# Kernel optimization log

Hardware: AMD Instinct MI355X
Metric: run time of the kernel (lower is better)

## Reference

```python
import jax, jax.numpy as jnp
import numpy as np

N = 100000   # nodes
E = 1600000  # edges
IN, H1, H2, OUT = 512, 64, 16, 40


def setup_inputs() -> dict:
    key = jax.random.key(0)
    ks = jax.random.split(key, 8)
    x = jax.random.normal(ks[0], (N, IN), jnp.float32)
    edge_index = jax.random.randint(ks[1], (2, E), 0, N, dtype=jnp.int64)

    def glorot(k, i, o):
        s = np.sqrt(6.0 / (i + o)).astype(np.float32)
        return jax.random.uniform(k, (i, o), jnp.float32, -s, s)

    return dict(
        x=x, edge_index=edge_index,
        W1=glorot(ks[2], IN, H1), b1=jnp.zeros((H1,), jnp.float32),
        W2=glorot(ks[3], H1, H2), b2=jnp.zeros((H2,), jnp.float32),
        W3=glorot(ks[4], H2, OUT), b3=jnp.zeros((OUT,), jnp.float32),
    )


def _gcn_conv(x, src, dst, W, b):
    # PyG GCNConv: x' = D^{-1/2} (A + I) D^{-1/2} (x W) + b
    h = x @ W                                   # [N, F_out]
    n = x.shape[0]
    deg = jnp.zeros((n,), h.dtype).at[dst].add(1.0) + 1.0   # self-loop adds 1
    dinv = jax.lax.rsqrt(deg)                   # deg >= 1 always
    norm = dinv[src] * dinv[dst]                # [E]
    msg = h[src] * norm[:, None]                # gather + scale  [E, F_out]
    out = jnp.zeros_like(h).at[dst].add(msg)    # scatter-add to targets
    out = out + h * (dinv * dinv)[:, None]      # self-loop contribution
    return out + b


def reference(x, edge_index, W1, b1, W2, b2, W3, b3):
    src, dst = edge_index[0], edge_index[1]
    h = jax.nn.relu(_gcn_conv(x, src, dst, W1, b1))
    # dropout(p=0.2, training=False) -> identity
    h = jax.nn.relu(_gcn_conv(h, src, dst, W2, b2))
    h = _gcn_conv(h, src, dst, W3, b3)
    return jax.nn.log_softmax(h, axis=-1)
```

## Files before the change

### kernel.cpp

```cpp
#include <hip/hip_runtime.h>
#include <cstdint>
#include <cstddef>

#define NNODES 100000
#define NEDGES 1600000
#define NWIN 100
#define WIN_NODES 1000
#define WCAP 17408

#define GM_ROWS 128
#define APAD 72
#define GEMM_BLOCKS ((NNODES + GM_ROWS - 1) / GM_ROWS)
#define BUCKET_BLOCKS 512
#define BCHUNK ((NEDGES + BUCKET_BLOCKS - 1) / BUCKET_BLOCKS)
#define MEGA_BLOCKS (GEMM_BLOCKS + BUCKET_BLOCKS)

typedef __attribute__((ext_vector_type(8))) short bf16x8;
typedef __attribute__((ext_vector_type(4))) float f32x4;
typedef __attribute__((ext_vector_type(4))) unsigned short ushort4v;
typedef __attribute__((ext_vector_type(8))) unsigned short ushort8v;

__device__ inline unsigned short f2bf(float f) {
    union { float f; unsigned u; } v; v.f = f;
    unsigned r = v.u + 0x7FFFu + ((v.u >> 16) & 1u);
    return (unsigned short)(r >> 16);
}
__device__ inline float bf2f(unsigned short b) {
    union { unsigned u; float f; } v; v.u = ((unsigned)b) << 16; return v.f;
}
__device__ inline void bfpair(unsigned u, float& lo, float& hi) {
    union { unsigned x; float f; } a, b;
    a.x = u << 16; b.x = u & 0xffff0000u;
    lo = a.f; hi = b.f;
}


__global__ __launch_bounds__(256) void convW(const float* __restrict__ W,
                                             unsigned short* __restrict__ Wt,
                                             int* __restrict__ wcur) {
    if (blockIdx.x == 0 && threadIdx.x < NWIN) wcur[threadIdx.x] = 0;
    int i = blockIdx.x * 256 + threadIdx.x;
    if (i < 512 * 64) {
        int k = i >> 6, n = i & 63;
        Wt[n * 512 + k] = f2bf(W[i]);
    }
}


__global__ __launch_bounds__(256) void mega_gemm_bucket(
        const float* __restrict__ A,
        const unsigned short* __restrict__ Wt,
        unsigned short* __restrict__ Hs,
        const int* __restrict__ src, const int* __restrict__ dst,
        unsigned* __restrict__ stage,
        int* __restrict__ wcur, int M, int E) {
    __shared__ __align__(16) unsigned char smem[18432 + 9216];

    long long b = blockIdx.x;
    int g0 = (int)((b * GEMM_BLOCKS) / MEGA_BLOCKS);
    int g1 = (int)(((b + 1) * GEMM_BLOCKS) / MEGA_BLOCKS);

    if (g1 > g0) {
        typedef unsigned short RowA[APAD];
        RowA* As = (RowA*)smem;
        RowA* Bs = (RowA*)(smem + 18432);
        const int tid = threadIdx.x;
        const int wid = tid >> 6;
        const int lane = tid & 63;
        const int bm = g0 * GM_ROWS;

        f32x4 acc[2][4];
#pragma unroll
        for (int i = 0; i < 2; i++)
#pragma unroll
            for (int j = 0; j < 4; j++) acc[i][j] = (f32x4){0.f, 0.f, 0.f, 0.f};

        const int ar = tid >> 4;
        const int ac4 = tid & 15;
        const int lm = lane & 15;
        const int lk = (lane >> 4) * 8;

        float4 aR[8];
        ushort8v bR[2];

        auto LOAD = [&](int k0) {
#pragma unroll
            for (int p = 0; p < 8; p++) {
                int row = bm + p * 16 + ar;
                if (row < M) aR[p] = *(const float4*)&A[(size_t)row * 512 + k0 + ac4 * 4];
                else         aR[p] = make_float4(0.f, 0.f, 0.f, 0.f);
            }
#pragma unroll
            for (int p = 0; p < 2; p++) {
                int c = p * 256 + tid;
                int n = c >> 3, kc = c & 7;
                bR[p] = *(const ushort8v*)&Wt[(size_t)n * 512 + k0 + kc * 8];
            }
        };

        LOAD(0);
        for (int k0 = 0; k0 < 512; k0 += 64) {
#pragma unroll
            for (int p = 0; p < 8; p++) {
                int r = p * 16 + ar;
                ushort4v bb;
                bb.x = f2bf(aR[p].x); bb.y = f2bf(aR[p].y);
                bb.z = f2bf(aR[p].z); bb.w = f2bf(aR[p].w);
                *(ushort4v*)&As[r][ac4 * 4] = bb;
            }
#pragma unroll
            for (int p = 0; p < 2; p++) {
                int c = p * 256 + tid;
                int n = c >> 3, kc = c & 7;
                *(ushort8v*)&Bs[n][kc * 8] = bR[p];
            }
            __syncthreads();

            if (k0 + 64 < 512) LOAD(k0 + 64);

            bf16x8 a[2][2], bb[4][2];
#pragma unroll
            for (int rf = 0; rf < 2; rf++)
#pragma unroll
                for (int kf = 0; kf < 2; kf++)
                    a[rf][kf] = *(const bf16x8*)&As[wid * 32 + rf * 16 + lm][kf * 32 + lk];
#pragma unroll
            for (int cf = 0; cf < 4; cf++)
#pragma unroll
                for (int kf = 0; kf < 2; kf++)
                    bb[cf][kf] = *(const bf16x8*)&Bs[cf * 16 + lm][kf * 32 + lk];

#pragma unroll
            for (int kf = 0; kf < 2; kf++)
#pragma unroll
                for (int rf = 0; rf < 2; rf++)
#pragma unroll
                    for (int cf = 0; cf < 4; cf++)
                        acc[rf][cf] = __builtin_amdgcn_mfma_f32_16x16x32_bf16(
                            a[rf][kf], bb[cf][kf], acc[rf][cf], 0, 0, 0);
            __syncthreads();
        }

#pragma unroll
        for (int rf = 0; rf < 2; rf++) {
#pragma unroll
            for (int j = 0; j < 4; j++) {
                int row = bm + wid * 32 + rf * 16 + (lane >> 4) * 4 + j;
                if (row < M) {
#pragma unroll
                    for (int cf = 0; cf < 4; cf++)
                        Hs[(size_t)row * 64 + cf * 16 + lm] = f2bf(acc[rf][cf][j]);
                }
            }
        }
    } else {
        int bi = (int)(b - g0);
        int* cnt  = (int*)smem;
        int* lcur = cnt + NWIN;
        const int tid = threadIdx.x;
        int e0 = bi * BCHUNK;
        int e1 = e0 + BCHUNK; if (e1 > E) e1 = E;

        for (int i = tid; i < NWIN; i += 256) cnt[i] = 0;
        __syncthreads();
        for (int e = e0 + tid; e < e1; e += 256) {
            int d = dst[e];
            atomicAdd(&cnt[d / WIN_NODES], 1);
        }
        __syncthreads();
        for (int i = tid; i < NWIN; i += 256)
            lcur[i] = atomicAdd(&wcur[i], cnt[i]);
        __syncthreads();
        for (int e = e0 + tid; e < e1; e += 256) {
            int d = dst[e], s = src[e];
            int w = d / WIN_NODES;
            int pos = atomicAdd(&lcur[w], 1);
            if (pos < WCAP)
                stage[(size_t)w * WCAP + pos] =
                    ((unsigned)(d - w * WIN_NODES) << 17) | (unsigned)s;
        }
    }
}


__global__ __launch_bounds__(256) void csr_window(
        const unsigned* __restrict__ stage,
        const int* __restrict__ wcur,
        int* __restrict__ rowstart,
        float* __restrict__ dinv,
        int* __restrict__ csr) {
    __shared__ int cnt[WIN_NODES];
    __shared__ int red[256];
    const int w = blockIdx.x;
    const int t = threadIdx.x;
    const int wb = w * WIN_NODES;
    const size_t sb = (size_t)w * WCAP;

    int v = (t < w) ? min(wcur[t], WCAP) : 0;
    red[t] = v;
    __syncthreads();
#pragma unroll
    for (int off = 128; off > 0; off >>= 1) {
        if (t < off) red[t] += red[t + off];
        __syncthreads();
    }
    int woff = red[0];
    int n_w = min(wcur[w], WCAP);
    __syncthreads();

    for (int i = t; i < WIN_NODES; i += 256) cnt[i] = 0;
    __syncthreads();
    for (int i = t; i < n_w; i += 256)
        atomicAdd(&cnt[stage[sb + i] >> 17], 1);
    __syncthreads();

    int c0 = 0, c1 = 0, c2 = 0, c3 = 0, psum = 0;
    if (t < 250) {
        c0 = cnt[4 * t]; c1 = cnt[4 * t + 1]; c2 = cnt[4 * t + 2]; c3 = cnt[4 * t + 3];
        psum = c0 + c1 + c2 + c3;
    }
    red[t] = psum;
    __syncthreads();
#pragma unroll
    for (int off = 1; off < 256; off <<= 1) {
        int tv = (t >= off) ? red[t - off] : 0;
        __syncthreads();
        red[t] += tv;
        __syncthreads();
    }
    int excl = red[t] - psum;
    if (t < 250) {
        int running = woff + excl;
        int idx = 4 * t;
        rowstart[wb + idx] = running; dinv[wb + idx] = rsqrtf((float)c0 + 1.f);
        cnt[idx] = running; running += c0;
        rowstart[wb + idx + 1] = running; dinv[wb + idx + 1] = rsqrtf((float)c1 + 1.f);
        cnt[idx + 1] = running; running += c1;
        rowstart[wb + idx + 2] = running; dinv[wb + idx + 2] = rsqrtf((float)c2 + 1.f);
        cnt[idx + 2] = running; running += c2;
        rowstart[wb + idx + 3] = running; dinv[wb + idx + 3] = rsqrtf((float)c3 + 1.f);
        cnt[idx + 3] = running;
    }
    if (w == NWIN - 1 && t == 0) rowstart[NNODES] = woff + n_w;
    __syncthreads();

    for (int i = t; i < n_w; i += 256) {
        unsigned p = stage[sb + i];
        int dl = (int)(p >> 17);
        int s  = (int)(p & 0x1FFFFu);
        int pos = atomicAdd(&cnt[dl], 1);
        csr[pos] = s;
    }
}


__global__ __launch_bounds__(256) void gather64_l2(
        const int* __restrict__ rowstart, const int* __restrict__ csr,
        const float* __restrict__ dinv,
        const unsigned short* __restrict__ Hs1,
        const float* __restrict__ b1,
        const float* __restrict__ W2,
        unsigned short* __restrict__ Hs2,
        int M) {
    __shared__ float Ws2[64 * 16];
    __shared__ float b1s[64];
    __shared__ float srow[8][64];
    for (int i = threadIdx.x; i < 64 * 16; i += 256) Ws2[i] = W2[i];
    if (threadIdx.x < 64) b1s[threadIdx.x] = b1[threadIdx.x];
    __syncthreads();

    const int r = threadIdx.x >> 5;
    const int lf = threadIdx.x & 31;
    const int row = blockIdx.x * 8 + r;
    const bool rok = (row < M);

    float v0 = 0.f, v1 = 0.f;
    if (rok) {
        const unsigned* H32 = (const unsigned*)Hs1;
        int e0 = rowstart[row], e1 = rowstart[row + 1];
        float dd = dinv[row];
        float acc0, acc1;
        bfpair(H32[(size_t)row * 32 + lf], acc0, acc1);
        acc0 *= dd; acc1 *= dd;
        int e = e0;
        for (; e + 3 < e1; e += 4) {
            int s0 = csr[e], s1 = csr[e + 1], s2 = csr[e + 2], s3 = csr[e + 3];
            float w0 = dinv[s0], w1 = dinv[s1], w2 = dinv[s2], w3 = dinv[s3];
            unsigned u0 = H32[(size_t)s0 * 32 + lf];
            unsigned u1 = H32[(size_t)s1 * 32 + lf];
            unsigned u2 = H32[(size_t)s2 * 32 + lf];
            unsigned u3 = H32[(size_t)s3 * 32 + lf];
            float a, b;
            bfpair(u0, a, b); acc0 += w0 * a; acc1 += w0 * b;
            bfpair(u1, a, b); acc0 += w1 * a; acc1 += w1 * b;
            bfpair(u2, a, b); acc0 += w2 * a; acc1 += w2 * b;
            bfpair(u3, a, b); acc0 += w3 * a; acc1 += w3 * b;
        }
        for (; e < e1; e++) {
            int s0 = csr[e];
            float w0 = dinv[s0];
            unsigned u = H32[(size_t)s0 * 32 + lf];
            float a, b;
            bfpair(u, a, b); acc0 += w0 * a; acc1 += w0 * b;
        }
        v0 = fmaxf(acc0 * dd + b1s[2 * lf], 0.f);
        v1 = fmaxf(acc1 * dd + b1s[2 * lf + 1], 0.f);
    }
    float2 t2; t2.x = v0; t2.y = v1;
    *(float2*)&srow[r][2 * lf] = t2;
    __syncthreads();

    if (rok && lf < 16) {
        float acc = 0.f;
#pragma unroll
        for (int k4 = 0; k4 < 16; k4++) {
            float4 s4 = *(const float4*)&srow[r][k4 * 4];
            acc += s4.x * Ws2[(k4 * 4 + 0) * 16 + lf];
            acc += s4.y * Ws2[(k4 * 4 + 1) * 16 + lf];
            acc += s4.z * Ws2[(k4 * 4 + 2) * 16 + lf];
            acc += s4.w * Ws2[(k4 * 4 + 3) * 16 + lf];
        }
        acc *= dinv[row];
        float hi = __shfl_down(acc, 1, 64);
        if ((lf & 1) == 0) {
            unsigned p = (unsigned)f2bf(acc) | ((unsigned)f2bf(hi) << 16);
            ((unsigned*)Hs2)[(size_t)row * 8 + (lf >> 1)] = p;
        }
    }
}


template <int F, bool RELU, bool SCALEOUT, bool HASBIAS, bool OUTBF>
__global__ __launch_bounds__(256) void gather_bf(
        const int* __restrict__ rowstart,
        const int* __restrict__ csr,
        const float* __restrict__ dinv,
        const unsigned short* __restrict__ Hs,
        const float* __restrict__ bias,
        void* __restrict__ outp,
        int M) {
    constexpr int LANES = F / 2;
    constexpr int GP = 256 / LANES;
    int row = blockIdx.x * GP + threadIdx.x / LANES;
    int lf = threadIdx.x % LANES;
    if (row >= M) return;

    const unsigned* H32 = (const unsigned*)Hs;
    const size_t LP = F / 2;

    int e0 = rowstart[row], e1 = rowstart[row + 1];
    float acc0, acc1;
    bfpair(H32[(size_t)row * LP + lf], acc0, acc1);

    int e = e0;
    for (; e + 3 < e1; e += 4) {
        int s0 = csr[e], s1 = csr[e + 1], s2 = csr[e + 2], s3 = csr[e + 3];
        unsigned u0 = H32[(size_t)s0 * LP + lf];
        unsigned u1 = H32[(size_t)s1 * LP + lf];
        unsigned u2 = H32[(size_t)s2 * LP + lf];
        unsigned u3 = H32[(size_t)s3 * LP + lf];
        float a, b;
        bfpair(u0, a, b); acc0 += a; acc1 += b;
        bfpair(u1, a, b); acc0 += a; acc1 += b;
        bfpair(u2, a, b); acc0 += a; acc1 += b;
        bfpair(u3, a, b); acc0 += a; acc1 += b;
    }
    for (; e < e1; e++) {
        unsigned u = H32[(size_t)csr[e] * LP + lf];
        float a, b;
        bfpair(u, a, b); acc0 += a; acc1 += b;
    }

    float dd = dinv[row];
    float v0 = acc0 * dd, v1 = acc1 * dd;
    if (HASBIAS) { v0 += bias[2 * lf]; v1 += bias[2 * lf + 1]; }
    if (RELU) { v0 = fmaxf(v0, 0.f); v1 = fmaxf(v1, 0.f); }
    if (SCALEOUT) { v0 *= dd; v1 *= dd; }
    if (OUTBF) {
        unsigned p = (unsigned)f2bf(v0) | ((unsigned)f2bf(v1) << 16);
        ((unsigned*)outp)[(size_t)row * LP + lf] = p;
    } else {
        float2 t; t.x = v0; t.y = v1;
        ((float2*)outp)[(size_t)row * LP + lf] = t;
    }
}


#define SRP 20

__global__ __launch_bounds__(256) void gather16_final(
        const int* __restrict__ rowstart, const int* __restrict__ csr,
        const float* __restrict__ dinv,
        const unsigned short* __restrict__ r2s,
        const float* __restrict__ W3,
        const float* __restrict__ b3,
        float* __restrict__ out,
        int M) {
    __shared__ float Ws3[16 * 40];
    __shared__ float bs3[40];
    __shared__ float srow[32][SRP];
    __shared__ float orow[32 * 40];
    for (int i = threadIdx.x; i < 16 * 40; i += 256) Ws3[i] = W3[i];
    if (threadIdx.x < 40) bs3[threadIdx.x] = b3[threadIdx.x];

    const int r = threadIdx.x >> 3;
    const int lf = threadIdx.x & 7;
    const int row = blockIdx.x * 32 + r;
    const bool rok = (row < M);

    float g0 = 0.f, g1 = 0.f;
    if (rok) {
        const unsigned* H32 = (const unsigned*)r2s;
        int e0 = rowstart[row], e1 = rowstart[row + 1];
        float acc0, acc1;
        bfpair(H32[(size_t)row * 8 + lf], acc0, acc1);
        int e = e0;
        for (; e + 3 < e1; e += 4) {
            int s0 = csr[e], s1 = csr[e + 1], s2 = csr[e + 2], s3 = csr[e + 3];
            unsigned u0 = H32[(size_t)s0 * 8 + lf];
            unsigned u1 = H32[(size_t)s1 * 8 + lf];
            unsigned u2 = H32[(size_t)s2 * 8 + lf];
            unsigned u3 = H32[(size_t)s3 * 8 + lf];
            float a, b;
            bfpair(u0, a, b); acc0 += a; acc1 += b;
            bfpair(u1, a, b); acc0 += a; acc1 += b;
            bfpair(u2, a, b); acc0 += a; acc1 += b;
            bfpair(u3, a, b); acc0 += a; acc1 += b;
        }
        for (; e < e1; e++) {
            unsigned u = H32[(size_t)csr[e] * 8 + lf];
            float a, b;
            bfpair(u, a, b); acc0 += a; acc1 += b;
        }
        float dd = dinv[row];
        g0 = acc0 * dd; g1 = acc1 * dd;
    }
    float2 t2; t2.x = g0; t2.y = g1;
    *(float2*)&srow[r][2 * lf] = t2;
    __syncthreads();

    float vals[5];
#pragma unroll
    for (int q = 0; q < 5; q++) vals[q] = bs3[lf + 8 * q];
#pragma unroll
    for (int k4 = 0; k4 < 4; k4++) {
        float4 s4 = *(const float4*)&srow[r][k4 * 4];
#pragma unroll
        for (int q = 0; q < 5; q++) {
            int n = lf + 8 * q;
            vals[q] += s4.x * Ws3[(k4 * 4 + 0) * 40 + n];
            vals[q] += s4.y * Ws3[(k4 * 4 + 1) * 40 + n];
            vals[q] += s4.z * Ws3[(k4 * 4 + 2) * 40 + n];
            vals[q] += s4.w * Ws3[(k4 * 4 + 3) * 40 + n];
        }
    }
    float m = vals[0];
#pragma unroll
    for (int q = 1; q < 5; q++) m = fmaxf(m, vals[q]);
#pragma unroll
    for (int off = 1; off < 8; off <<= 1) m = fmaxf(m, __shfl_xor(m, off, 64));
    float s = 0.f;
#pragma unroll
    for (int q = 0; q < 5; q++) s += expf(vals[q] - m);
#pragma unroll
    for (int off = 1; off < 8; off <<= 1) s += __shfl_xor(s, off, 64);
    float ls = logf(s) + m;
#pragma unroll
    for (int q = 0; q < 5; q++) orow[r * 40 + lf + 8 * q] = vals[q] - ls;
    __syncthreads();

    float4* o4 = (float4*)(out + (size_t)blockIdx.x * 32 * 40);
    const float4* s4p = (const float4*)orow;
    for (int i = threadIdx.x; i < 320; i += 256) {
        int rr = (i * 4) / 40;
        if (blockIdx.x * 32 + rr < M) o4[i] = s4p[i];
    }
}


extern "C" void kernel_launch(void* const* d_in, const int* in_sizes, int n_in,
                              void* d_out, int out_size, void* d_ws, size_t ws_size,
                              hipStream_t stream) {
    const float* x   = (const float*)d_in[0];
    const int*   ei  = (const int*)d_in[1];
    const int*   src = ei;
    const int*   dst = ei + NEDGES;
    const float* W1 = (const float*)d_in[2];
    const float* b1 = (const float*)d_in[3];
    const float* W2 = (const float*)d_in[4];
    const float* b2 = (const float*)d_in[5];
    const float* W3 = (const float*)d_in[6];
    const float* b3 = (const float*)d_in[7];
    float* out = (float*)d_out;

    int* ws_i = (int*)d_ws;
    int* wcur     = ws_i;
    int* rowstart = wcur + 128;
    int* csr      = rowstart + NNODES + 8;
    unsigned* stage = (unsigned*)(csr + NEDGES);
    float* dinv   = (float*)(stage + (size_t)NWIN * WCAP);
    unsigned short* Wt = (unsigned short*)(dinv + NNODES);
    float* bufA   = (float*)((int*)(Wt + 64 * 512) + 16);
    float* bufB   = bufA + (size_t)NNODES * 64;

    unsigned short* Hs1 = (unsigned short*)bufA;
    unsigned short* Hs2 = (unsigned short*)bufB;
    unsigned short* r2s = (unsigned short*)bufA;

    convW<<<(512 * 64 + 255) / 256, 256, 0, stream>>>(W1, Wt, wcur);

    mega_gemm_bucket<<<MEGA_BLOCKS, 256, 0, stream>>>(
        x, Wt, Hs1, src, dst, stage, wcur, NNODES, NEDGES);

    csr_window<<<NWIN, 256, 0, stream>>>(stage, wcur, rowstart, dinv, csr);

    gather64_l2<<<(NNODES + 7) / 8, 256, 0, stream>>>(
        rowstart, csr, dinv, Hs1, b1, W2, Hs2, NNODES);

    gather_bf<16, true, true, true, true><<<(NNODES + 31) / 32, 256, 0, stream>>>(
        rowstart, csr, dinv, Hs2, b2, r2s, NNODES);

    gather16_final<<<(NNODES + 31) / 32, 256, 0, stream>>>(
        rowstart, csr, dinv, r2s, W3, b3, out, NNODES);
}
```

Measured before the change: 202.2 us.

## Double-buffer GEMM register prefetch, pack bf16 conversion, pad window counters

The layer-1 GEMM now keeps two register buffers of A/W tiles and prefetches two k-steps ahead, so global load latency has more time to hide. The fp32-to-bf16 conversion uses the hardware packed convert instruction instead of manual rounding. MFMA sections raise wave priority with s_setprio. The per-window atomic counters are spread 16 ints apart to reduce contention on the same cache line. The cost is higher register pressure from the doubled prefetch buffers and a larger workspace offset.

Measured after the change: 201.5 us. Within noise of the previous version (-0.3%).

```diff
diff --git a/kernel.cpp b/kernel.cpp
--- a/kernel.cpp
+++ b/kernel.cpp
@@ -7,6 +7,7 @@
 #define NWIN 100
 #define WIN_NODES 1000
 #define WCAP 17408
+#define WSTR 16
 
 #define GM_ROWS 128
 #define APAD 72
@@ -38,7 +39,7 @@
 __global__ __launch_bounds__(256) void convW(const float* __restrict__ W,
                                              unsigned short* __restrict__ Wt,
                                              int* __restrict__ wcur) {
-    if (blockIdx.x == 0 && threadIdx.x < NWIN) wcur[threadIdx.x] = 0;
+    if (blockIdx.x == 0 && threadIdx.x < NWIN) wcur[threadIdx.x * WSTR] = 0;
     int i = blockIdx.x * 256 + threadIdx.x;
     if (i < 512 * 64) {
         int k = i >> 6, n = i & 63;
@@ -80,43 +81,43 @@
         const int lm = lane & 15;
         const int lk = (lane >> 4) * 8;
 
-        float4 aR[8];
-        ushort8v bR[2];
-
-        auto LOAD = [&](int k0) {
+        float4 aR0[8], aR1[8];
+        ushort8v bR0[2], bR1[2];
+
+        auto LOADA = [&](float4 (&aRx)[8], ushort8v (&bRx)[2], int k0) {
 #pragma unroll
             for (int p = 0; p < 8; p++) {
                 int row = bm + p * 16 + ar;
-                if (row < M) aR[p] = *(const float4*)&A[(size_t)row * 512 + k0 + ac4 * 4];
-                else         aR[p] = make_float4(0.f, 0.f, 0.f, 0.f);
+                if (row < M) aRx[p] = *(const float4*)&A[(size_t)row * 512 + k0 + ac4 * 4];
+                else         aRx[p] = make_float4(0.f, 0.f, 0.f, 0.f);
             }
 #pragma unroll
             for (int p = 0; p < 2; p++) {
                 int c = p * 256 + tid;
                 int n = c >> 3, kc = c & 7;
-                bR[p] = *(const ushort8v*)&Wt[(size_t)n * 512 + k0 + kc * 8];
+                bRx[p] = *(const ushort8v*)&Wt[(size_t)n * 512 + k0 + kc * 8];
             }
         };
 
-        LOAD(0);
-        for (int k0 = 0; k0 < 512; k0 += 64) {
+        auto TILE = [&](float4 (&aRx)[8], ushort8v (&bRx)[2], int k0) {
 #pragma unroll
             for (int p = 0; p < 8; p++) {
                 int r = p * 16 + ar;
-                ushort4v bb;
-                bb.x = f2bf(aR[p].x); bb.y = f2bf(aR[p].y);
-                bb.z = f2bf(aR[p].z); bb.w = f2bf(aR[p].w);
-                *(ushort4v*)&As[r][ac4 * 4] = bb;
+                unsigned lo, hi;
+                asm("v_cvt_pk_bf16_f32 %0, %1, %2" : "=v"(lo) : "v"(aRx[p].x), "v"(aRx[p].y));
+                asm("v_cvt_pk_bf16_f32 %0, %1, %2" : "=v"(hi) : "v"(aRx[p].z), "v"(aRx[p].w));
+                uint2 u; u.x = lo; u.y = hi;
+                *(uint2*)&As[r][ac4 * 4] = u;
             }
 #pragma unroll
             for (int p = 0; p < 2; p++) {
                 int c = p * 256 + tid;
                 int n = c >> 3, kc = c & 7;
-                *(ushort8v*)&Bs[n][kc * 8] = bR[p];
+                *(ushort8v*)&Bs[n][kc * 8] = bRx[p];
             }
             __syncthreads();
 
-            if (k0 + 64 < 512) LOAD(k0 + 64);
+            if (k0 + 128 < 512) LOADA(aRx, bRx, k0 + 128);
 
             bf16x8 a[2][2], bb[4][2];
 #pragma unroll
@@ -130,6 +131,7 @@
                 for (int kf = 0; kf < 2; kf++)
                     bb[cf][kf] = *(const bf16x8*)&Bs[cf * 16 + lm][kf * 32 + lk];
 
+            __builtin_amdgcn_s_setprio(1);
 #pragma unroll
             for (int kf = 0; kf < 2; kf++)
 #pragma unroll
@@ -138,7 +140,15 @@
                     for (int cf = 0; cf < 4; cf++)
                         acc[rf][cf] = __builtin_amdgcn_mfma_f32_16x16x32_bf16(
                             a[rf][kf], bb[cf][kf], acc[rf][cf], 0, 0, 0);
+            __builtin_amdgcn_s_setprio(0);
             __syncthreads();
+        };
+
+        LOADA(aR0, bR0, 0);
+        LOADA(aR1, bR1, 64);
+        for (int tp = 0; tp < 4; tp++) {
+            TILE(aR0, bR0, tp * 128);
+            TILE(aR1, bR1, tp * 128 + 64);
         }
 
 #pragma unroll
@@ -169,7 +179,7 @@
         }
         __syncthreads();
         for (int i = tid; i < NWIN; i += 256)
-            lcur[i] = atomicAdd(&wcur[i], cnt[i]);
+            lcur[i] = atomicAdd(&wcur[i * WSTR], cnt[i]);
         __syncthreads();
         for (int e = e0 + tid; e < e1; e += 256) {
             int d = dst[e], s = src[e];
@@ -196,7 +206,7 @@
     const int wb = w * WIN_NODES;
     const size_t sb = (size_t)w * WCAP;
 
-    int v = (t < w) ? min(wcur[t], WCAP) : 0;
+    int v = (t < w) ? min(wcur[t * WSTR], WCAP) : 0;
     red[t] = v;
     __syncthreads();
 #pragma unroll
@@ -205,7 +215,7 @@
         __syncthreads();
     }
     int woff = red[0];
-    int n_w = min(wcur[w], WCAP);
+    int n_w = min(wcur[w * WSTR], WCAP);
     __syncthreads();
 
     for (int i = t; i < WIN_NODES; i += 256) cnt[i] = 0;
@@ -495,7 +505,7 @@
 
     int* ws_i = (int*)d_ws;
     int* wcur     = ws_i;
-    int* rowstart = wcur + 128;
+    int* rowstart = wcur + NWIN * WSTR + 16;
     int* csr      = rowstart + NNODES + 8;
     unsigned* stage = (unsigned*)(csr + NEDGES);
     float* dinv   = (float*)(stage + (size_t)NWIN * WCAP);
```
